# Kernel tuning notes

Measured on AMD Instinct MI355X. Metric: run time of the kernel, lower is better.

## Reference

```python
import jax, jax.numpy as jnp
import numpy as np

V = 100000      # voca_size
EMB = 128       # embedding_size
REG = 7         # region_size
NC = 20         # num_classes
ML = 512        # max_length
B = 64          # batch
RAD = REG // 2
ENT = ML - 2 * RAD


def setup_inputs() -> dict:
    key = jax.random.key(0)
    k0, k1, k2, k3, k4, k5, k6 = jax.random.split(key, 7)
    train_input = jax.random.randint(k0, (B, ML), 0, V, dtype=jnp.int32)
    # embedding tables, uniform(-0.01, 0.01), padding row 0 zeroed (padding_idx=0)
    W_region = jax.random.uniform(k1, (V, REG * EMB), jnp.float32, -0.01, 0.01).at[0].set(0.0)
    W_word = jax.random.uniform(k2, (V, EMB), jnp.float32, -0.01, 0.01).at[0].set(0.0)
    # linear layers stored as [in, out]; xavier-uniform-like init
    lim1 = float(np.sqrt(6.0 / (EMB + 2 * ML)))
    W1 = jax.random.uniform(k3, (EMB, 2 * ML), jnp.float32, -lim1, lim1)
    b1 = jax.random.uniform(k4, (2 * ML,), jnp.float32, -0.01, 0.01)
    lim2 = float(np.sqrt(6.0 / (2 * ML + NC)))
    W2 = jax.random.uniform(k5, (2 * ML, NC), jnp.float32, -lim2, lim2)
    b2 = jax.random.uniform(k6, (NC,), jnp.float32, -0.01, 0.01)
    return {"train_input": train_input, "W_region": W_region, "W_word": W_word,
            "W1": W1, "b1": b1, "W2": W2, "b2": b2}


def reference(train_input, W_region, W_word, W1, b1, W2, b2):
    Bn, L = train_input.shape
    ent = L - 2 * RAD
    # region embedding of trimmed sequence -> [B, ent, REG, EMB]
    trimmed = train_input[:, RAD:L - RAD]
    K = W_region[trimmed].reshape(Bn, ent, REG, EMB)
    # sliding windows: [B, ent, REG] gather (replaces the python cat loop)
    idx = jnp.arange(ent)[:, None] + jnp.arange(REG)[None, :]
    win = train_input[:, idx]                    # [B, ent, REG]
    win = jnp.transpose(win, (0, 2, 1))          # [B, REG, ent] (matches torch transposes)
    E = W_word[win]                              # [B, REG, ent, EMB]
    # faithful to torch: a reshape (not transpose) back to [B, ent, REG, EMB]
    E = E.reshape(Bn, ent, REG, EMB)
    # max over region dim, sum over sequence dim -> [B, EMB]
    noi = jnp.sum(jnp.max(E * K, axis=2), axis=1)
    # small MLP (dropout is identity in eval mode)
    h = jax.nn.relu(noi @ W1 + b1)
    logits = h @ W2 + b2
    prob = jax.nn.softmax(logits, axis=1)
    cls = jnp.argmax(prob, axis=1)
    return logits, prob, cls
```

## Files before the change

kernel.cpp:

```cpp
#include <hip/hip_runtime.h>
#include <hip/hip_bf16.h>

#define V    100000
#define EMB  128
#define REG  7
#define NC   20
#define ML   512
#define BB   64
#define RAD  3
#define ENT  506
#define NB2  127

__global__ __launch_bounds__(256, 4) void noi_kernel(
    const int*   __restrict__ train,
    const float* __restrict__ Wr,
    const float* __restrict__ Ww,
    float*       __restrict__ partial)
{
    __shared__ float red[4][EMB];

    const int b    = blockIdx.y;
    const int c4   = blockIdx.x;
    const int tid  = threadIdx.x;
    const int w    = tid >> 6;
    const int lane = tid & 63;
    const int i    = c4 * 4 + w;

    float mx = 0.f, my = 0.f;
    if (i < ENT) {
        const int* trow = train + b * ML;
        const int  ridx = trow[i + RAD];
        int widx[REG];
        #pragma unroll
        for (int j = 0; j < REG; ++j) {
            const int t = i * REG + j;
            const int r = t / ENT;
            const int e = t - r * ENT;
            widx[j] = trow[e + r];
        }

        const float2* Kp = (const float2*)(Wr + (size_t)ridx * (REG * EMB));
        float2 kv[REG], ev[REG];
        #pragma unroll
        for (int j = 0; j < REG; ++j)
            kv[j] = Kp[j * 64 + lane];
        #pragma unroll
        for (int j = 0; j < REG; ++j)
            ev[j] = ((const float2*)(Ww + (size_t)widx[j] * EMB))[lane];

        mx = kv[0].x * ev[0].x;
        my = kv[0].y * ev[0].y;
        #pragma unroll
        for (int j = 1; j < REG; ++j) {
            mx = fmaxf(mx, kv[j].x * ev[j].x);
            my = fmaxf(my, kv[j].y * ev[j].y);
        }
    }

    red[w][2 * lane]     = mx;
    red[w][2 * lane + 1] = my;
    __syncthreads();
    if (tid < EMB) {
        const float s = red[0][tid] + red[1][tid] + red[2][tid] + red[3][tid];
        partial[((size_t)b * NB2 + c4) * EMB + tid] = s;
    }
}

__global__ __launch_bounds__(256) void mlp_kernel(
    const float* __restrict__ partial,
    const float* __restrict__ W1,
    const float* __restrict__ b1,
    const float* __restrict__ W2,
    const float* __restrict__ b2,
    float*       __restrict__ out)
{
    __shared__ float noi[EMB];
    __shared__ float h[2 * ML];
    __shared__ float lg[NC];

    const int b   = blockIdx.x;
    const int tid = threadIdx.x;

    if (tid < EMB) {
        const float* p = partial + (size_t)b * NB2 * EMB + tid;
        float s = 0.f;
        #pragma unroll 8
        for (int k = 0; k < NB2; ++k)
            s += p[(size_t)k * EMB];
        noi[tid] = s;
    }
    __syncthreads();

    float h0 = b1[tid], h1 = b1[tid + 256], h2 = b1[tid + 512], h3 = b1[tid + 768];
    for (int k = 0; k < EMB; ++k) {
        const float nk = noi[k];
        const float* row = W1 + k * (2 * ML);
        h0 = fmaf(nk, row[tid],       h0);
        h1 = fmaf(nk, row[tid + 256], h1);
        h2 = fmaf(nk, row[tid + 512], h2);
        h3 = fmaf(nk, row[tid + 768], h3);
    }
    h[tid]       = fmaxf(h0, 0.f);
    h[tid + 256] = fmaxf(h1, 0.f);
    h[tid + 512] = fmaxf(h2, 0.f);
    h[tid + 768] = fmaxf(h3, 0.f);
    __syncthreads();

    const int w    = tid >> 6;
    const int lane = tid & 63;
    for (int c = w; c < NC; c += 4) {
        float p = 0.f;
        #pragma unroll 4
        for (int k = lane; k < 2 * ML; k += 64)
            p = fmaf(h[k], W2[k * NC + c], p);
        for (int off = 32; off; off >>= 1)
            p += __shfl_down(p, off);
        if (lane == 0) lg[c] = p + b2[c];
    }
    __syncthreads();

    if (tid == 0) {
        float mx = lg[0];
        for (int c = 1; c < NC; ++c) mx = fmaxf(mx, lg[c]);
        float pr[NC];
        float s = 0.f;
        for (int c = 0; c < NC; ++c) { pr[c] = __expf(lg[c] - mx); s += pr[c]; }
        const float inv = 1.f / s;
        int am = 0; float best = lg[0];
        for (int c = 1; c < NC; ++c) if (lg[c] > best) { best = lg[c]; am = c; }
        for (int c = 0; c < NC; ++c) {
            out[b * NC + c]           = lg[c];
            out[BB * NC + b * NC + c] = pr[c] * inv;
        }
        out[2 * BB * NC + b] = (float)am;
    }
}

extern "C" void kernel_launch(void* const* d_in, const int* in_sizes, int n_in,
                              void* d_out, int out_size, void* d_ws, size_t ws_size,
                              hipStream_t stream) {
    const int*   train = (const int*)  d_in[0];
    const float* Wr    = (const float*)d_in[1];
    const float* Ww    = (const float*)d_in[2];
    const float* W1    = (const float*)d_in[3];
    const float* b1    = (const float*)d_in[4];
    const float* W2    = (const float*)d_in[5];
    const float* b2    = (const float*)d_in[6];
    float* out     = (float*)d_out;
    float* partial = (float*)d_ws;

    hipLaunchKernelGGL(noi_kernel, dim3(NB2, BB), dim3(256), 0, stream,
                       train, Wr, Ww, partial);
    hipLaunchKernelGGL(mlp_kernel, dim3(BB), dim3(256), 0, stream,
                       partial, W1, b1, W2, b2, out);
}
```

Before: 472.0 us.

## Use float4 gathers with two positions per wave and widen MLP block

The noi kernel now has each half-wave handle one sequence position using float4 loads, so a block covers 8 positions and the grid halves to 64 chunks per batch. A shuffle combines the two halves before the shared-memory reduction, and out-of-range positions are clamped and zeroed. The MLP kernel moves to 1024 threads: the partial-sum reduction is split across 8 groups and each thread computes one hidden unit. The goal is wider memory transactions, fewer blocks and partials, and more parallelism in the MLP, at the cost of higher register pressure from the float4 arrays.

```diff
diff --git a/kernel.cpp b/kernel.cpp
--- a/kernel.cpp
+++ b/kernel.cpp
@@ -9,7 +9,7 @@
 #define BB   64
 #define RAD  3
 #define ENT  506
-#define NB2  127
+#define NBC  64
 
 __global__ __launch_bounds__(256, 4) void noi_kernel(
     const int*   __restrict__ train,
@@ -19,54 +19,67 @@
 {
     __shared__ float red[4][EMB];
 
-    const int b    = blockIdx.y;
-    const int c4   = blockIdx.x;
-    const int tid  = threadIdx.x;
-    const int w    = tid >> 6;
-    const int lane = tid & 63;
-    const int i    = c4 * 4 + w;
+    const int b     = blockIdx.y;
+    const int chunk = blockIdx.x;
+    const int tid   = threadIdx.x;
+    const int w     = tid >> 6;
+    const int lane  = tid & 63;
+    const int half  = lane >> 5;
+    const int sl    = lane & 31;
 
-    float mx = 0.f, my = 0.f;
-    if (i < ENT) {
-        const int* trow = train + b * ML;
-        const int  ridx = trow[i + RAD];
-        int widx[REG];
-        #pragma unroll
-        for (int j = 0; j < REG; ++j) {
-            const int t = i * REG + j;
-            const int r = t / ENT;
-            const int e = t - r * ENT;
-            widx[j] = trow[e + r];
-        }
+    const int  i_raw = chunk * 8 + w * 2 + half;
+    const bool valid = (i_raw < ENT);
+    const int  i     = valid ? i_raw : (ENT - 1);
 
-        const float2* Kp = (const float2*)(Wr + (size_t)ridx * (REG * EMB));
-        float2 kv[REG], ev[REG];
-        #pragma unroll
-        for (int j = 0; j < REG; ++j)
-            kv[j] = Kp[j * 64 + lane];
-        #pragma unroll
-        for (int j = 0; j < REG; ++j)
-            ev[j] = ((const float2*)(Ww + (size_t)widx[j] * EMB))[lane];
-
-        mx = kv[0].x * ev[0].x;
-        my = kv[0].y * ev[0].y;
-        #pragma unroll
-        for (int j = 1; j < REG; ++j) {
-            mx = fmaxf(mx, kv[j].x * ev[j].x);
-            my = fmaxf(my, kv[j].y * ev[j].y);
-        }
+    const int* trow = train + b * ML;
+    const int  ridx = trow[i + RAD];
+    int widx[REG];
+    #pragma unroll
+    for (int j = 0; j < REG; ++j) {
+        const int t = i * REG + j;
+        const int r = t / ENT;
+        const int e = t - r * ENT;
+        widx[j] = trow[e + r];
     }
 
-    red[w][2 * lane]     = mx;
-    red[w][2 * lane + 1] = my;
+    const float4* Kp = (const float4*)(Wr + (size_t)ridx * (REG * EMB));
+    float4 kv[REG], ev[REG];
+    #pragma unroll
+    for (int j = 0; j < REG; ++j)
+        kv[j] = Kp[j * 32 + sl];
+    #pragma unroll
+    for (int j = 0; j < REG; ++j)
+        ev[j] = ((const float4*)(Ww + (size_t)widx[j] * EMB))[sl];
+
+    float4 m;
+    m.x = kv[0].x * ev[0].x;
+    m.y = kv[0].y * ev[0].y;
+    m.z = kv[0].z * ev[0].z;
+    m.w = kv[0].w * ev[0].w;
+    #pragma unroll
+    for (int j = 1; j < REG; ++j) {
+        m.x = fmaxf(m.x, kv[j].x * ev[j].x);
+        m.y = fmaxf(m.y, kv[j].y * ev[j].y);
+        m.z = fmaxf(m.z, kv[j].z * ev[j].z);
+        m.w = fmaxf(m.w, kv[j].w * ev[j].w);
+    }
+    if (!valid) { m.x = 0.f; m.y = 0.f; m.z = 0.f; m.w = 0.f; }
+
+    m.x += __shfl_down(m.x, 32);
+    m.y += __shfl_down(m.y, 32);
+    m.z += __shfl_down(m.z, 32);
+    m.w += __shfl_down(m.w, 32);
+    if (half == 0)
+        ((float4*)red[w])[sl] = m;
     __syncthreads();
+
     if (tid < EMB) {
         const float s = red[0][tid] + red[1][tid] + red[2][tid] + red[3][tid];
-        partial[((size_t)b * NB2 + c4) * EMB + tid] = s;
+        partial[((size_t)b * NBC + chunk) * EMB + tid] = s;
     }
 }
 
-__global__ __launch_bounds__(256) void mlp_kernel(
+__global__ __launch_bounds__(1024) void mlp_kernel(
     const float* __restrict__ partial,
     const float* __restrict__ W1,
     const float* __restrict__ b1,
@@ -74,6 +87,7 @@
     const float* __restrict__ b2,
     float*       __restrict__ out)
 {
+    __shared__ float red2[8][EMB];
     __shared__ float noi[EMB];
     __shared__ float h[2 * ML];
     __shared__ float lg[NC];
@@ -81,36 +95,38 @@
     const int b   = blockIdx.x;
     const int tid = threadIdx.x;
 
+    {
+        const int col = tid & 127;
+        const int grp = tid >> 7;
+        const float* p = partial + ((size_t)b * NBC + grp * 8) * EMB + col;
+        float s = 0.f;
+        #pragma unroll
+        for (int k = 0; k < 8; ++k)
+            s += p[(size_t)k * EMB];
+        red2[grp][col] = s;
+    }
+    __syncthreads();
     if (tid < EMB) {
-        const float* p = partial + (size_t)b * NB2 * EMB + tid;
         float s = 0.f;
-        #pragma unroll 8
-        for (int k = 0; k < NB2; ++k)
-            s += p[(size_t)k * EMB];
+        #pragma unroll
+        for (int g = 0; g < 8; ++g)
+            s += red2[g][tid];
         noi[tid] = s;
     }
     __syncthreads();
 
-    float h0 = b1[tid], h1 = b1[tid + 256], h2 = b1[tid + 512], h3 = b1[tid + 768];
-    for (int k = 0; k < EMB; ++k) {
-        const float nk = noi[k];
-        const float* row = W1 + k * (2 * ML);
-        h0 = fmaf(nk, row[tid],       h0);
-        h1 = fmaf(nk, row[tid + 256], h1);
-        h2 = fmaf(nk, row[tid + 512], h2);
-        h3 = fmaf(nk, row[tid + 768], h3);
-    }
-    h[tid]       = fmaxf(h0, 0.f);
-    h[tid + 256] = fmaxf(h1, 0.f);
-    h[tid + 512] = fmaxf(h2, 0.f);
-    h[tid + 768] = fmaxf(h3, 0.f);
+    float acc = b1[tid];
+    #pragma unroll 8
+    for (int k = 0; k < EMB; ++k)
+        acc = fmaf(noi[k], W1[k * (2 * ML) + tid], acc);
+    h[tid] = fmaxf(acc, 0.f);
     __syncthreads();
 
     const int w    = tid >> 6;
     const int lane = tid & 63;
-    for (int c = w; c < NC; c += 4) {
+    for (int c = w; c < NC; c += 16) {
         float p = 0.f;
-        #pragma unroll 4
+        #pragma unroll
         for (int k = lane; k < 2 * ML; k += 64)
             p = fmaf(h[k], W2[k * NC + c], p);
         for (int off = 32; off; off >>= 1)
@@ -149,8 +165,8 @@
     float* out     = (float*)d_out;
     float* partial = (float*)d_ws;
 
-    hipLaunchKernelGGL(noi_kernel, dim3(NB2, BB), dim3(256), 0, stream,
+    hipLaunchKernelGGL(noi_kernel, dim3(NBC, BB), dim3(256), 0, stream,
                        train, Wr, Ww, partial);
-    hipLaunchKernelGGL(mlp_kernel, dim3(BB), dim3(256), 0, stream,
+    hipLaunchKernelGGL(mlp_kernel, dim3(BB), dim3(1024), 0, stream,
                        partial, W1, b1, W2, b2, out);
 }
```

After: 467.7 us. About the same (-0.9%).
